# Optimization experiments

Hardware: AMD Instinct MI355X
Metric: run time of the kernel (lower is better)

## Reference

```python
import jax, jax.numpy as jnp
import numpy as np
import math

V, S, D, B = 50257, 2048, 512, 4
DFF = 4 * D
EPS = 1e-5


def layer_norm(z, g, b):
    mu = jnp.mean(z, axis=-1, keepdims=True)
    var = jnp.mean((z - mu) ** 2, axis=-1, keepdims=True)
    return (z - mu) * jax.lax.rsqrt(var + EPS) * g + b


def pos_embedding(seq_len, d_model):
    # Faithful to get_positional_value: angle = pos / 10000**(2*i/d), sin for even i, cos for odd i
    pos = jnp.arange(seq_len, dtype=jnp.float32)[:, None]          # [S,1]
    i = jnp.arange(d_model, dtype=jnp.float32)[None, :]            # [1,D]
    ang = pos / jnp.power(10000.0, 2.0 * i / d_model)              # [S,D]
    even = (jnp.arange(d_model) % 2 == 0)[None, :]
    return jnp.where(even, jnp.sin(ang), jnp.cos(ang))


def setup_inputs() -> dict:
    key = jax.random.key(0)
    ks = jax.random.split(key, 14)
    w = lambda k, sh: jax.random.normal(k, sh, dtype=jnp.float32) * 0.02
    return {
        "input_seq": jax.random.randint(ks[0], (B, S), 0, V),
        "emb": w(ks[1], (V, D)),
        "wk": w(ks[2], (D, D)), "bk": jnp.zeros((D,), jnp.float32),
        "wq": w(ks[3], (D, D)), "bq": jnp.zeros((D,), jnp.float32),
        "wv": w(ks[4], (D, D)), "bv": jnp.zeros((D,), jnp.float32),
        "ln_g": jnp.ones((D,), jnp.float32), "ln_b": jnp.zeros((D,), jnp.float32),
        "w1": w(ks[5], (D, DFF)), "b1": jnp.zeros((DFF,), jnp.float32),
        "w2": w(ks[6], (DFF, D)), "b2": jnp.zeros((D,), jnp.float32),
    }


def reference(input_seq, emb, wk, bk, wq, bq, wv, bv, ln_g, ln_b, w1, b1, w2, b2):
    x = emb[input_seq]                                              # [B,S,D]
    x = (x + pos_embedding(S, D)) * math.sqrt(D)
    # NB original passes (k, q, v) into Attention(Q, K, V), so Q:=k_proj, K:=q_proj, V:=v_proj
    k = x @ wk + bk
    q = x @ wq + bq
    v = x @ wv + bv
    scores = jnp.einsum("bid,bjd->bij", k, q) / math.sqrt(D)        # [B,S,S]
    attn = jax.nn.softmax(scores, axis=-1) @ v                      # [B,S,D]
    r = layer_norm(x + attn, ln_g, ln_b)
    ff = jax.nn.gelu(r @ w1 + b1, approximate=False) @ w2 + b2
    out = layer_norm(r + ff, ln_g, ln_b)                            # shared LN params (same module reused)
    return out
```

## Files before the change

kernel.cpp:

```cpp
#include <hip/hip_runtime.h>
#include <math.h>

static constexpr int BB  = 4;
static constexpr int S   = 2048;
static constexpr int D   = 512;
static constexpr int DFF = 2048;
static constexpr int BS  = BB * S;

using v8h = __attribute__((ext_vector_type(8))) _Float16;
using v4h = __attribute__((ext_vector_type(4))) _Float16;
using v2h = __attribute__((ext_vector_type(2))) _Float16;
using v4f = __attribute__((ext_vector_type(4))) float;

__device__ __forceinline__ void async16(const void* g, void* l) {
  __builtin_amdgcn_global_load_lds(
      (const __attribute__((address_space(1))) unsigned int*)g,
      (__attribute__((address_space(3))) unsigned int*)l, 16, 0, 0);
}

__device__ __forceinline__ void xcd_swizzle(int& bx, int& by) {
  const int nx = gridDim.x;
  const int nwg = nx * gridDim.y;
  const int lin = by * nx + bx;
  const int q = nwg >> 3;
  const int nl = (lin & 7) * q + (lin >> 3);
  bx = nl % nx;
  by = nl / nx;
}

__device__ __forceinline__ float fast_gelu(float v) {
  const float u = 0.7071067811865476f * v;
  const float a = fabsf(u);
  const float t = 1.0f / (1.0f + 0.3275911f * a);
  const float p =
      t * (0.254829592f +
           t * (-0.284496736f +
                t * (1.421413741f + t * (-1.453152027f + t * 1.061405429f))));
  const float e = exp2f(-u * u * 1.4426950408889634f);
  const float erfv = copysignf(1.0f - p * e, u);
  return 0.5f * v * (1.0f + erfv);
}

__device__ __forceinline__ float blockSum(float v) {
#pragma unroll
  for (int o = 32; o; o >>= 1) v += __shfl_xor(v, o, 64);
  __shared__ float t[4];
  __syncthreads();
  if ((threadIdx.x & 63) == 0) t[threadIdx.x >> 6] = v;
  __syncthreads();
  return t[0] + t[1] + t[2] + t[3];
}
__device__ __forceinline__ float blockMax(float v) {
#pragma unroll
  for (int o = 32; o; o >>= 1) v = fmaxf(v, __shfl_xor(v, o, 64));
  __shared__ float t[4];
  __syncthreads();
  if ((threadIdx.x & 63) == 0) t[threadIdx.x >> 6] = v;
  __syncthreads();
  return fmaxf(fmaxf(t[0], t[1]), fmaxf(t[2], t[3]));
}

__global__ __launch_bounds__(256) void embed_pos_k(
    const int* __restrict__ seq, const float* __restrict__ emb,
    float* __restrict__ X, _Float16* __restrict__ Xh) {
  const int bs = blockIdx.x;
  const int s  = bs & (S - 1);
  const int idx = seq[bs];
  const float* er = emb + (size_t)idx * D;
  const float cexp = -0.05190512648261504f;
  const int d0 = threadIdx.x * 2;
  const float2 e2 = *(const float2*)&er[d0];
  const float a0 = (float)s * exp2f((float)d0 * cexp);
  const float a1 = (float)s * exp2f((float)(d0 + 1) * cexp);
  const float v0 = (e2.x + sinf(a0)) * 22.62741699796952f;
  const float v1 = (e2.y + cosf(a1)) * 22.62741699796952f;
  const size_t o = (size_t)bs * D + d0;
  *(float2*)&X[o] = make_float2(v0, v1);
  *(v2h*)&Xh[o] = v2h{(_Float16)v0, (_Float16)v1};
}

__global__ __launch_bounds__(256) void prep_k(
    const float* __restrict__ wk, const float* __restrict__ wq,
    const float* __restrict__ wv, const float* __restrict__ w1,
    const float* __restrict__ w2, const float* __restrict__ bk,
    const float* __restrict__ bq, const float* __restrict__ bv,
    _Float16* __restrict__ wcat, _Float16* __restrict__ w1T,
    _Float16* __restrict__ w2T, float* __restrict__ bcat) {
  const int idx = blockIdx.x * 256 + threadIdx.x;
  if (idx < 786432) {
    const int which = idx >> 18, e = idx & 262143;
    const int k = e >> 9, n = e & 511;
    const float* w = (which == 0) ? wk : (which == 1) ? wq : wv;
    wcat[((long)(which * 512 + n)) * 512 + k] = (_Float16)w[e];
  } else if (idx < 786432 + 1048576) {
    const int e = idx - 786432;
    const int k = e >> 11, n = e & 2047;
    w1T[(long)n * 512 + k] = (_Float16)w1[e];
  } else if (idx < 786432 + 2097152) {
    const int e = idx - 786432 - 1048576;
    const int k = e >> 9, n = e & 511;
    w2T[(long)n * 2048 + k] = (_Float16)w2[e];
  } else if (idx < 786432 + 2097152 + 1536) {
    const int e = idx - 786432 - 2097152;
    const float* b = (e < 512) ? bk : (e < 1024) ? bq : bv;
    bcat[e] = b[e & 511];
  }
}

template <int OMODE, int ACT>
__global__ __launch_bounds__(256) void mm32_k(
    const _Float16* __restrict__ Ap, const _Float16* __restrict__ Bp,
    void* __restrict__ Cp, void* __restrict__ Cp2, void* __restrict__ Cp3,
    const float* __restrict__ bias,
    int N, int K, long sA, long sB, long sC, float scale) {
  constexpr int ATE = 128 * 32;
  constexpr int TILE = 2 * ATE;
  __shared__ __align__(16) _Float16 lds[2 * TILE];

  const int tid = threadIdx.x, lane = tid & 63, w = tid >> 6;
  const int quad = lane >> 4, l16 = lane & 15;
  const int wm = w >> 1, wn = w & 1;
  int bx = blockIdx.x, by = blockIdx.y;
  xcd_swizzle(bx, by);
  const int m0 = by * 128, n0 = bx * 128;

  const _Float16* A = Ap + (long)blockIdx.z * sA;
  const _Float16* B = Bp + (long)blockIdx.z * sB;

  v4f acc[4][4] = {};
  const int rloc = lane >> 2;
  const int cs = (lane & 3) ^ ((rloc >> 1) & 3);

  auto stage = [&](int k0, int half) {
    _Float16* Ah = lds + half * TILE;
    _Float16* Bh = Ah + ATE;
#pragma unroll
    for (int i = 0; i < 2; ++i) {
      const int is = w + i * 4;
      async16(A + (long)(m0 + is * 16 + rloc) * K + k0 + cs * 8, Ah + is * 512);
      async16(B + (long)(n0 + is * 16 + rloc) * K + k0 + cs * 8, Bh + is * 512);
    }
  };

  stage(0, 0);
  __syncthreads();

  const int nK = K >> 5;
  for (int t = 0; t < nK; ++t) {
    const int cur = t & 1;
    if (t + 1 < nK) stage((t + 1) << 5, cur ^ 1);

    const _Float16* Ah = lds + cur * TILE;
    const _Float16* Bh = Ah + ATE;

    v8h af[4], bfr[4];
#pragma unroll
    for (int mt = 0; mt < 4; ++mt) {
      const int rr = wm * 64 + mt * 16 + l16;
      const int pc = quad ^ ((rr >> 1) & 3);
      af[mt] = *(v8h*)&Ah[rr * 32 + pc * 8];
    }
#pragma unroll
    for (int nt = 0; nt < 4; ++nt) {
      const int rn = wn * 64 + nt * 16 + l16;
      const int pc = quad ^ ((rn >> 1) & 3);
      bfr[nt] = *(v8h*)&Bh[rn * 32 + pc * 8];
    }
#pragma unroll
    for (int mt = 0; mt < 4; ++mt)
#pragma unroll
      for (int nt = 0; nt < 4; ++nt)
        acc[mt][nt] = __builtin_amdgcn_mfma_f32_16x16x32_f16(
            af[mt], bfr[nt], acc[mt][nt], 0, 0, 0);

    __syncthreads();
  }

  const long Cz = (long)blockIdx.z * sC;
  const int region = n0 >> 9;
#pragma unroll
  for (int nt = 0; nt < 4; ++nt) {
    const int gn = n0 + wn * 64 + nt * 16 + l16;
    const int gnl = gn & 511;
    const float bv = bias ? bias[gn] : 0.0f;
#pragma unroll
    for (int mt = 0; mt < 4; ++mt) {
      const int gmb = m0 + wm * 64 + mt * 16 + quad * 4;
      if constexpr (OMODE == 4) {
        if (region == 2) {
          const int z2 = gmb >> 11, ml = gmb & 2047;
          v4h h4;
#pragma unroll
          for (int r = 0; r < 4; ++r)
            h4[r] = (_Float16)(acc[mt][nt][r] * scale + bv);
          *(v4h*)&((_Float16*)Cp3)[((long)z2 * 512 + gnl) * 2048 + ml] = h4;
          continue;
        }
      }
#pragma unroll
      for (int r = 0; r < 4; ++r) {
        const int gm = gmb + r;
        float v = acc[mt][nt][r] * scale + bv;
        if constexpr (ACT == 1) v = fast_gelu(v);
        if constexpr (OMODE == 0) {
          ((float*)Cp)[Cz + (long)gm * N + gn] = v;
        } else if constexpr (OMODE == 1) {
          ((_Float16*)Cp)[Cz + (long)gm * N + gn] = (_Float16)v;
        } else {
          if (region == 0) {
            ((_Float16*)Cp)[(long)gm * 512 + gnl] = (_Float16)v;
          } else {
            ((_Float16*)Cp2)[(long)gm * 512 + gnl] = (_Float16)v;
          }
        }
      }
    }
  }
}

template <int TM, int OMODE, int ACT>
__global__ __launch_bounds__(256) void mm_k(
    const _Float16* __restrict__ Ap, const _Float16* __restrict__ Bp,
    void* __restrict__ Cp, void* __restrict__ Cp2, void* __restrict__ Cp3,
    const float* __restrict__ bias,
    int N, int K, long sA, long sB, long sC, float scale) {
  constexpr int ATE = TM * 64;
  constexpr int BTE = 128 * 64;
  constexpr int TILE = ATE + BTE;
  __shared__ __align__(16) _Float16 lds[2 * TILE];

  const int tid = threadIdx.x, lane = tid & 63, w = tid >> 6;
  const int quad = lane >> 4, l16 = lane & 15;
  constexpr int MT = 4;
  constexpr int NT = (TM == 128) ? 4 : 2;
  constexpr int WN = (TM == 128) ? 64 : 32;
  const int wm = (TM == 128) ? (w >> 1) : 0;
  const int wn = (TM == 128) ? (w & 1) : w;
  int bx = blockIdx.x, by = blockIdx.y;
  xcd_swizzle(bx, by);
  const int m0 = by * TM, n0 = bx * 128;

  const _Float16* A = Ap + (long)blockIdx.z * sA;
  const _Float16* B = Bp + (long)blockIdx.z * sB;

  v4f acc[MT][NT] = {};
  const int srow8 = lane >> 3;
  const int cs = (lane & 7) ^ srow8;
  const int lsw = l16 & 7;

  auto stage = [&](int k0, int half) {
    _Float16* Ah = lds + half * TILE;
    _Float16* Bh = Ah + ATE;
#pragma unroll
    for (int i = 0; i < TM / 32; ++i) {
      const int is = w + i * 4;
      async16(A + (long)(m0 + is * 8 + srow8) * K + k0 + cs * 8, Ah + is * 512);
    }
#pragma unroll
    for (int i = 0; i < 4; ++i) {
      const int is = w + i * 4;
      async16(B + (long)(n0 + is * 8 + srow8) * K + k0 + cs * 8, Bh + is * 512);
    }
  };

  stage(0, 0);
  __syncthreads();

  const int nK = K >> 6;
  for (int t = 0; t < nK; ++t) {
    const int cur = t & 1;
    if (t + 1 < nK) stage((t + 1) << 6, cur ^ 1);

    const _Float16* Ah = lds + cur * TILE;
    const _Float16* Bh = Ah + ATE;

    v8h af[MT][2], bfr[NT][2];
#pragma unroll
    for (int mt = 0; mt < MT; ++mt) {
      const int rr = wm * 64 + mt * 16 + l16;
#pragma unroll
      for (int kk = 0; kk < 2; ++kk) {
        const int c = (kk * 4 + quad) ^ lsw;
        af[mt][kk] = *(v8h*)&Ah[rr * 64 + c * 8];
      }
    }
#pragma unroll
    for (int nt = 0; nt < NT; ++nt) {
      const int rn = wn * WN + nt * 16 + l16;
#pragma unroll
      for (int kk = 0; kk < 2; ++kk) {
        const int c = (kk * 4 + quad) ^ lsw;
        bfr[nt][kk] = *(v8h*)&Bh[rn * 64 + c * 8];
      }
    }
#pragma unroll
    for (int kk = 0; kk < 2; ++kk)
#pragma unroll
      for (int mt = 0; mt < MT; ++mt)
#pragma unroll
        for (int nt = 0; nt < NT; ++nt)
          acc[mt][nt] = __builtin_amdgcn_mfma_f32_16x16x32_f16(
              af[mt][kk], bfr[nt][kk], acc[mt][nt], 0, 0, 0);

    __syncthreads();
  }

  const long Cz = (long)blockIdx.z * sC;
#pragma unroll
  for (int nt = 0; nt < NT; ++nt) {
    const int gn = n0 + wn * WN + nt * 16 + l16;
    const float bv = bias ? bias[gn] : 0.0f;
#pragma unroll
    for (int mt = 0; mt < MT; ++mt) {
      const int gmb = m0 + wm * 64 + mt * 16 + quad * 4;
#pragma unroll
      for (int r = 0; r < 4; ++r) {
        const int gm = gmb + r;
        float v = acc[mt][nt][r] * scale + bv;
        if constexpr (ACT == 1) v = fast_gelu(v);
        if constexpr (OMODE == 0) {
          ((float*)Cp)[Cz + (long)gm * N + gn] = v;
        } else {
          ((_Float16*)Cp)[Cz + (long)gm * N + gn] = (_Float16)v;
        }
      }
    }
  }
}

__global__ __launch_bounds__(256) void mm64p_k(
    const _Float16* __restrict__ Ap, const _Float16* __restrict__ Bp,
    float* __restrict__ Cp, const float* __restrict__ bias,
    int N, int K, long sA, long sB, long sC, float scale) {
  constexpr int ATE = 64 * 64;
  constexpr int BTE = 128 * 64;
  constexpr int TILE = ATE + BTE;
  __shared__ __align__(16) _Float16 lds[3 * TILE];

  const int tid = threadIdx.x, lane = tid & 63, w = tid >> 6;
  const int quad = lane >> 4, l16 = lane & 15;
  int bx = blockIdx.x, by = blockIdx.y;
  xcd_swizzle(bx, by);
  const int m0 = by * 64, n0 = bx * 128;

  const _Float16* A = Ap + (long)blockIdx.z * sA;
  const _Float16* B = Bp + (long)blockIdx.z * sB;

  v4f acc[4][2] = {};
  const int srow8 = lane >> 3;
  const int cs = (lane & 7) ^ srow8;
  const int lsw = l16 & 7;

  auto stage = [&](int t) {
    _Float16* Ah = lds + (t % 3) * TILE;
    _Float16* Bh = Ah + ATE;
    const int k0 = t << 6;
#pragma unroll
    for (int i = 0; i < 2; ++i) {
      const int is = w + i * 4;
      async16(A + (long)(m0 + is * 8 + srow8) * K + k0 + cs * 8, Ah + is * 512);
    }
#pragma unroll
    for (int i = 0; i < 4; ++i) {
      const int is = w + i * 4;
      async16(B + (long)(n0 + is * 8 + srow8) * K + k0 + cs * 8, Bh + is * 512);
    }
  };

  const int nK = K >> 6;
  stage(0);
  stage(1);

  for (int t = 0; t < nK; ++t) {
    __builtin_amdgcn_s_barrier();
    if (t + 2 < nK) {
      stage(t + 2);
      asm volatile("s_waitcnt vmcnt(12)" ::: "memory");
    } else if (t + 1 < nK) {
      asm volatile("s_waitcnt vmcnt(6)" ::: "memory");
    } else {
      asm volatile("s_waitcnt vmcnt(0)" ::: "memory");
    }
    __builtin_amdgcn_s_barrier();

    const _Float16* Ah = lds + (t % 3) * TILE;
    const _Float16* Bh = Ah + ATE;

    v8h af[4][2], bfr[2][2];
#pragma unroll
    for (int mt = 0; mt < 4; ++mt) {
      const int rr = mt * 16 + l16;
#pragma unroll
      for (int kk = 0; kk < 2; ++kk) {
        const int c = (kk * 4 + quad) ^ lsw;
        af[mt][kk] = *(v8h*)&Ah[rr * 64 + c * 8];
      }
    }
#pragma unroll
    for (int nt = 0; nt < 2; ++nt) {
      const int rn = w * 32 + nt * 16 + l16;
#pragma unroll
      for (int kk = 0; kk < 2; ++kk) {
        const int c = (kk * 4 + quad) ^ lsw;
        bfr[nt][kk] = *(v8h*)&Bh[rn * 64 + c * 8];
      }
    }
#pragma unroll
    for (int kk = 0; kk < 2; ++kk)
#pragma unroll
      for (int mt = 0; mt < 4; ++mt)
#pragma unroll
        for (int nt = 0; nt < 2; ++nt)
          acc[mt][nt] = __builtin_amdgcn_mfma_f32_16x16x32_f16(
              af[mt][kk], bfr[nt][kk], acc[mt][nt], 0, 0, 0);
  }

  const long Cz = (long)blockIdx.z * sC;
#pragma unroll
  for (int nt = 0; nt < 2; ++nt) {
    const int gn = n0 + w * 32 + nt * 16 + l16;
    const float bv = bias ? bias[gn] : 0.0f;
#pragma unroll
    for (int mt = 0; mt < 4; ++mt) {
      const int gmb = m0 + mt * 16 + quad * 4;
#pragma unroll
      for (int r = 0; r < 4; ++r) {
        const int gm = gmb + r;
        Cp[Cz + (long)gm * N + gn] = acc[mt][nt][r] * scale + bv;
      }
    }
  }
}

__global__ __launch_bounds__(256) void softmax_k(_Float16* __restrict__ Sc) {
  _Float16* p = Sc + (size_t)blockIdx.x * S;
  const int base = threadIdx.x * 8;
  const v8h a = *(const v8h*)(p + base);
  float v[8];
#pragma unroll
  for (int i = 0; i < 8; ++i) v[i] = (float)a[i];
  float m = -1e30f;
#pragma unroll
  for (int i = 0; i < 8; ++i) m = fmaxf(m, v[i]);
  m = blockMax(m);
  float sum = 0.f;
#pragma unroll
  for (int i = 0; i < 8; ++i) {
    v[i] = exp2f((v[i] - m) * 1.44269504f);
    sum += v[i];
  }
  sum = blockSum(sum);
  const float inv = 1.0f / sum;
  v8h o;
#pragma unroll
  for (int i = 0; i < 8; ++i) o[i] = (_Float16)(v[i] * inv);
  *(v8h*)(p + base) = o;
}

__global__ __launch_bounds__(256) void ln_res_k(
    float* __restrict__ X, const float* __restrict__ Add,
    const float* __restrict__ g, const float* __restrict__ b,
    _Float16* __restrict__ rF) {
  float* xr = X + (size_t)blockIdx.x * D;
  const float* ar = Add + (size_t)blockIdx.x * D;
  _Float16* rf = rF + (size_t)blockIdx.x * D;
  const int d0 = threadIdx.x * 2;
  const float2 xv = *(const float2*)&xr[d0];
  const float2 av = *(const float2*)&ar[d0];
  const float z0 = xv.x + av.x;
  const float z1 = xv.y + av.y;
  const float mu = blockSum(z0 + z1) * (1.0f / D);
  const float dd0 = z0 - mu, dd1 = z1 - mu;
  const float var = blockSum(dd0 * dd0 + dd1 * dd1) * (1.0f / D);
  const float rs = rsqrtf(var + 1e-5f);
  const float2 gv = *(const float2*)&g[d0];
  const float2 bv = *(const float2*)&b[d0];
  const float v0 = dd0 * rs * gv.x + bv.x;
  const float v1 = dd1 * rs * gv.y + bv.y;
  *(float2*)&xr[d0] = make_float2(v0, v1);
  *(v2h*)&rf[d0] = v2h{(_Float16)v0, (_Float16)v1};
}

__global__ __launch_bounds__(256) void ln_out_k(
    const float* __restrict__ R, const float* __restrict__ F,
    const float* __restrict__ g, const float* __restrict__ b,
    float* __restrict__ out) {
  const float* rr = R + (size_t)blockIdx.x * D;
  const float* fr = F + (size_t)blockIdx.x * D;
  float* orow = out + (size_t)blockIdx.x * D;
  const int d0 = threadIdx.x * 2;
  const float2 rv = *(const float2*)&rr[d0];
  const float2 fv = *(const float2*)&fr[d0];
  const float z0 = rv.x + fv.x;
  const float z1 = rv.y + fv.y;
  const float mu = blockSum(z0 + z1) * (1.0f / D);
  const float dd0 = z0 - mu, dd1 = z1 - mu;
  const float var = blockSum(dd0 * dd0 + dd1 * dd1) * (1.0f / D);
  const float rs = rsqrtf(var + 1e-5f);
  const float2 gv = *(const float2*)&g[d0];
  const float2 bv = *(const float2*)&b[d0];
  *(float2*)&orow[d0] =
      make_float2(dd0 * rs * gv.x + bv.x, dd1 * rs * gv.y + bv.y);
}

extern "C" void kernel_launch(void* const* d_in, const int* in_sizes, int n_in,
                              void* d_out, int out_size, void* d_ws, size_t ws_size,
                              hipStream_t stream) {
  (void)in_sizes; (void)n_in; (void)out_size; (void)ws_size;
  const int*   seq = (const int*)d_in[0];
  const float* emb = (const float*)d_in[1];
  const float* wk  = (const float*)d_in[2];
  const float* bk  = (const float*)d_in[3];
  const float* wq  = (const float*)d_in[4];
  const float* bq  = (const float*)d_in[5];
  const float* wv  = (const float*)d_in[6];
  const float* bv  = (const float*)d_in[7];
  const float* lng = (const float*)d_in[8];
  const float* lnb = (const float*)d_in[9];
  const float* w1  = (const float*)d_in[10];
  const float* b1  = (const float*)d_in[11];
  const float* w2  = (const float*)d_in[12];
  const float* b2  = (const float*)d_in[13];

  const size_t MBy = 1024 * 1024;
  char* wsb = (char*)d_ws;
  float*    X    = (float*)wsb;
  _Float16* Xh   = (_Float16*)(wsb + 16 * MBy);
  _Float16* kF   = (_Float16*)(wsb + 24 * MBy);
  _Float16* qF   = (_Float16*)(wsb + 32 * MBy);
  _Float16* vT   = (_Float16*)(wsb + 40 * MBy);
  _Float16* Sc   = (_Float16*)(wsb + 48 * MBy);
  float*    attn = (float*)(wsb + 81 * MBy);
  _Float16* rF   = (_Float16*)(wsb + 24 * MBy);
  _Float16* hF   = (_Float16*)(wsb + 48 * MBy);
  float*    ff   = (float*)(wsb + 32 * MBy);
  _Float16* wcat = (_Float16*)(wsb + 100 * MBy);
  float*    bcat = (float*)(wsb + 102 * MBy);
  _Float16* w1T  = (_Float16*)(wsb + 103 * MBy);
  _Float16* w2T  = (_Float16*)(wsb + 105 * MBy);

  const long SD = (long)S * D, SSl = (long)S * S;

  prep_k<<<11270, 256, 0, stream>>>(wk, wq, wv, w1, w2, bk, bq, bv,
                                    wcat, w1T, w2T, bcat);
  embed_pos_k<<<BS, 256, 0, stream>>>(seq, emb, X, Xh);

  mm32_k<4, 0><<<dim3(12, 64, 1), 256, 0, stream>>>(
      Xh, wcat, kF, qF, vT, bcat, 1536, D, 0, 0, 0, 1.0f);

  mm32_k<1, 0><<<dim3(16, 16, BB), 256, 0, stream>>>(
      kF, qF, Sc, nullptr, nullptr, nullptr, S, D, SD, SD, SSl,
      0.044194173824159216f);

  softmax_k<<<BS, 256, 0, stream>>>(Sc);

  mm64p_k<<<dim3(4, 32, BB), 256, 0, stream>>>(
      Sc, vT, attn, nullptr, D, S, SSl, (long)D * S, SD, 1.0f);

  ln_res_k<<<BS, 256, 0, stream>>>(X, attn, lng, lnb, rF);

  mm32_k<1, 1><<<dim3(16, 64, 1), 256, 0, stream>>>(
      rF, w1T, hF, nullptr, nullptr, b1, DFF, D, 0, 0, 0, 1.0f);
  mm64p_k<<<dim3(4, 128, 1), 256, 0, stream>>>(
      hF, w2T, ff, b2, D, DFF, 0, 0, 0, 1.0f);

  ln_out_k<<<BS, 256, 0, stream>>>(X, ff, lng, lnb, (float*)d_out);
}
```

Before: 351.6 us.

## Fuse softmax into PV matmul with online max/sum rescaling

```diff
diff --git a/kernel.cpp b/kernel.cpp
--- a/kernel.cpp
+++ b/kernel.cpp
@@ -202,140 +202,31 @@
         const int gm = gmb + r;
         float v = acc[mt][nt][r] * scale + bv;
         if constexpr (ACT == 1) v = fast_gelu(v);
-        if constexpr (OMODE == 0) {
-          ((float*)Cp)[Cz + (long)gm * N + gn] = v;
-        } else if constexpr (OMODE == 1) {
+        if constexpr (OMODE == 1) {
           ((_Float16*)Cp)[Cz + (long)gm * N + gn] = (_Float16)v;
-        } else {
+        } else if constexpr (OMODE == 4) {
           if (region == 0) {
             ((_Float16*)Cp)[(long)gm * 512 + gnl] = (_Float16)v;
           } else {
             ((_Float16*)Cp2)[(long)gm * 512 + gnl] = (_Float16)v;
           }
+        } else {
+          ((float*)Cp)[Cz + (long)gm * N + gn] = v;
         }
       }
     }
   }
 }
 
-template <int TM, int OMODE, int ACT>
-__global__ __launch_bounds__(256) void mm_k(
+__global__ __launch_bounds__(256) void pv_sm_k(
     const _Float16* __restrict__ Ap, const _Float16* __restrict__ Bp,
-    void* __restrict__ Cp, void* __restrict__ Cp2, void* __restrict__ Cp3,
-    const float* __restrict__ bias,
-    int N, int K, long sA, long sB, long sC, float scale) {
-  constexpr int ATE = TM * 64;
-  constexpr int BTE = 128 * 64;
-  constexpr int TILE = ATE + BTE;
-  __shared__ __align__(16) _Float16 lds[2 * TILE];
-
-  const int tid = threadIdx.x, lane = tid & 63, w = tid >> 6;
-  const int quad = lane >> 4, l16 = lane & 15;
-  constexpr int MT = 4;
-  constexpr int NT = (TM == 128) ? 4 : 2;
-  constexpr int WN = (TM == 128) ? 64 : 32;
-  const int wm = (TM == 128) ? (w >> 1) : 0;
-  const int wn = (TM == 128) ? (w & 1) : w;
-  int bx = blockIdx.x, by = blockIdx.y;
-  xcd_swizzle(bx, by);
-  const int m0 = by * TM, n0 = bx * 128;
-
-  const _Float16* A = Ap + (long)blockIdx.z * sA;
-  const _Float16* B = Bp + (long)blockIdx.z * sB;
-
-  v4f acc[MT][NT] = {};
-  const int srow8 = lane >> 3;
-  const int cs = (lane & 7) ^ srow8;
-  const int lsw = l16 & 7;
-
-  auto stage = [&](int k0, int half) {
-    _Float16* Ah = lds + half * TILE;
-    _Float16* Bh = Ah + ATE;
-#pragma unroll
-    for (int i = 0; i < TM / 32; ++i) {
-      const int is = w + i * 4;
-      async16(A + (long)(m0 + is * 8 + srow8) * K + k0 + cs * 8, Ah + is * 512);
-    }
-#pragma unroll
-    for (int i = 0; i < 4; ++i) {
-      const int is = w + i * 4;
-      async16(B + (long)(n0 + is * 8 + srow8) * K + k0 + cs * 8, Bh + is * 512);
-    }
-  };
-
-  stage(0, 0);
-  __syncthreads();
-
-  const int nK = K >> 6;
-  for (int t = 0; t < nK; ++t) {
-    const int cur = t & 1;
-    if (t + 1 < nK) stage((t + 1) << 6, cur ^ 1);
-
-    const _Float16* Ah = lds + cur * TILE;
-    const _Float16* Bh = Ah + ATE;
-
-    v8h af[MT][2], bfr[NT][2];
-#pragma unroll
-    for (int mt = 0; mt < MT; ++mt) {
-      const int rr = wm * 64 + mt * 16 + l16;
-#pragma unroll
-      for (int kk = 0; kk < 2; ++kk) {
-        const int c = (kk * 4 + quad) ^ lsw;
-        af[mt][kk] = *(v8h*)&Ah[rr * 64 + c * 8];
-      }
-    }
-#pragma unroll
-    for (int nt = 0; nt < NT; ++nt) {
-      const int rn = wn * WN + nt * 16 + l16;
-#pragma unroll
-      for (int kk = 0; kk < 2; ++kk) {
-        const int c = (kk * 4 + quad) ^ lsw;
-        bfr[nt][kk] = *(v8h*)&Bh[rn * 64 + c * 8];
-      }
-    }
-#pragma unroll
-    for (int kk = 0; kk < 2; ++kk)
-#pragma unroll
-      for (int mt = 0; mt < MT; ++mt)
-#pragma unroll
-        for (int nt = 0; nt < NT; ++nt)
-          acc[mt][nt] = __builtin_amdgcn_mfma_f32_16x16x32_f16(
-              af[mt][kk], bfr[nt][kk], acc[mt][nt], 0, 0, 0);
-
-    __syncthreads();
-  }
-
-  const long Cz = (long)blockIdx.z * sC;
-#pragma unroll
-  for (int nt = 0; nt < NT; ++nt) {
-    const int gn = n0 + wn * WN + nt * 16 + l16;
-    const float bv = bias ? bias[gn] : 0.0f;
-#pragma unroll
-    for (int mt = 0; mt < MT; ++mt) {
-      const int gmb = m0 + wm * 64 + mt * 16 + quad * 4;
-#pragma unroll
-      for (int r = 0; r < 4; ++r) {
-        const int gm = gmb + r;
-        float v = acc[mt][nt][r] * scale + bv;
-        if constexpr (ACT == 1) v = fast_gelu(v);
-        if constexpr (OMODE == 0) {
-          ((float*)Cp)[Cz + (long)gm * N + gn] = v;
-        } else {
-          ((_Float16*)Cp)[Cz + (long)gm * N + gn] = (_Float16)v;
-        }
-      }
-    }
-  }
-}
-
-__global__ __launch_bounds__(256) void mm64p_k(
-    const _Float16* __restrict__ Ap, const _Float16* __restrict__ Bp,
-    float* __restrict__ Cp, const float* __restrict__ bias,
-    int N, int K, long sA, long sB, long sC, float scale) {
+    float* __restrict__ Cp,
+    int N, int K, long sA, long sB, long sC) {
   constexpr int ATE = 64 * 64;
   constexpr int BTE = 128 * 64;
   constexpr int TILE = ATE + BTE;
   __shared__ __align__(16) _Float16 lds[3 * TILE];
+  __shared__ __align__(16) float mS[64], lS[64], rS[64];
 
   const int tid = threadIdx.x, lane = tid & 63, w = tid >> 6;
   const int quad = lane >> 4, l16 = lane & 15;
@@ -346,10 +237,13 @@
   const _Float16* A = Ap + (long)blockIdx.z * sA;
   const _Float16* B = Bp + (long)blockIdx.z * sB;
 
+  if (tid < 64) { mS[tid] = -1e30f; lS[tid] = 0.0f; }
+
   v4f acc[4][2] = {};
   const int srow8 = lane >> 3;
   const int cs = (lane & 7) ^ srow8;
   const int lsw = l16 & 7;
+  const float L2E = 1.44269504f;
 
   auto stage = [&](int t) {
     _Float16* Ah = lds + (t % 3) * TILE;
@@ -405,6 +299,175 @@
         bfr[nt][kk] = *(v8h*)&Bh[rn * 64 + c * 8];
       }
     }
+
+    float tmax[4];
+#pragma unroll
+    for (int mt = 0; mt < 4; ++mt) {
+      float tm = -1e30f;
+#pragma unroll
+      for (int kk = 0; kk < 2; ++kk)
+#pragma unroll
+        for (int j = 0; j < 8; ++j)
+          tm = fmaxf(tm, (float)af[mt][kk][j]);
+      tm = fmaxf(tm, __shfl_xor(tm, 16, 64));
+      tm = fmaxf(tm, __shfl_xor(tm, 32, 64));
+      tmax[mt] = tm;
+    }
+    if (w == 0 && quad == 0) {
+#pragma unroll
+      for (int mt = 0; mt < 4; ++mt) {
+        const int rr = mt * 16 + l16;
+        const float mo = mS[rr];
+        const float mn = fmaxf(mo, tmax[mt]);
+        rS[rr] = exp2f((mo - mn) * L2E);
+        mS[rr] = mn;
+      }
+    }
+    asm volatile("s_waitcnt lgkmcnt(0)" ::: "memory");
+    __builtin_amdgcn_s_barrier();
+
+    v8h paf[4][2];
+    float ts[4];
+#pragma unroll
+    for (int mt = 0; mt < 4; ++mt) {
+      const int rr = mt * 16 + l16;
+      const float mn = mS[rr];
+      float s = 0.f;
+#pragma unroll
+      for (int kk = 0; kk < 2; ++kk)
+#pragma unroll
+        for (int j = 0; j < 8; ++j) {
+          const float p = exp2f(((float)af[mt][kk][j] - mn) * L2E);
+          s += p;
+          paf[mt][kk][j] = (_Float16)p;
+        }
+      s += __shfl_xor(s, 16, 64);
+      s += __shfl_xor(s, 32, 64);
+      ts[mt] = s;
+    }
+    if (w == 0 && quad == 0) {
+#pragma unroll
+      for (int mt = 0; mt < 4; ++mt) {
+        const int rr = mt * 16 + l16;
+        lS[rr] = lS[rr] * rS[rr] + ts[mt];
+      }
+    }
+
+#pragma unroll
+    for (int mt = 0; mt < 4; ++mt) {
+      const v4f r4 = *(const v4f*)&rS[mt * 16 + quad * 4];
+#pragma unroll
+      for (int nt = 0; nt < 2; ++nt)
+#pragma unroll
+        for (int r = 0; r < 4; ++r)
+          acc[mt][nt][r] *= r4[r];
+    }
+
+#pragma unroll
+    for (int kk = 0; kk < 2; ++kk)
+#pragma unroll
+      for (int mt = 0; mt < 4; ++mt)
+#pragma unroll
+        for (int nt = 0; nt < 2; ++nt)
+          acc[mt][nt] = __builtin_amdgcn_mfma_f32_16x16x32_f16(
+              paf[mt][kk], bfr[nt][kk], acc[mt][nt], 0, 0, 0);
+  }
+
+  asm volatile("s_waitcnt lgkmcnt(0)" ::: "memory");
+  __builtin_amdgcn_s_barrier();
+
+  const long Cz = (long)blockIdx.z * sC;
+#pragma unroll
+  for (int nt = 0; nt < 2; ++nt) {
+    const int gn = n0 + w * 32 + nt * 16 + l16;
+#pragma unroll
+    for (int mt = 0; mt < 4; ++mt) {
+      const int gmb = m0 + mt * 16 + quad * 4;
+      const v4f l4 = *(const v4f*)&lS[mt * 16 + quad * 4];
+#pragma unroll
+      for (int r = 0; r < 4; ++r)
+        Cp[Cz + (long)(gmb + r) * N + gn] = acc[mt][nt][r] / l4[r];
+    }
+  }
+}
+
+__global__ __launch_bounds__(256) void mm64p_k(
+    const _Float16* __restrict__ Ap, const _Float16* __restrict__ Bp,
+    float* __restrict__ Cp, const float* __restrict__ bias,
+    int N, int K, long sA, long sB, long sC, float scale) {
+  constexpr int ATE = 64 * 64;
+  constexpr int BTE = 128 * 64;
+  constexpr int TILE = ATE + BTE;
+  __shared__ __align__(16) _Float16 lds[3 * TILE];
+
+  const int tid = threadIdx.x, lane = tid & 63, w = tid >> 6;
+  const int quad = lane >> 4, l16 = lane & 15;
+  int bx = blockIdx.x, by = blockIdx.y;
+  xcd_swizzle(bx, by);
+  const int m0 = by * 64, n0 = bx * 128;
+
+  const _Float16* A = Ap + (long)blockIdx.z * sA;
+  const _Float16* B = Bp + (long)blockIdx.z * sB;
+
+  v4f acc[4][2] = {};
+  const int srow8 = lane >> 3;
+  const int cs = (lane & 7) ^ srow8;
+  const int lsw = l16 & 7;
+
+  auto stage = [&](int t) {
+    _Float16* Ah = lds + (t % 3) * TILE;
+    _Float16* Bh = Ah + ATE;
+    const int k0 = t << 6;
+#pragma unroll
+    for (int i = 0; i < 2; ++i) {
+      const int is = w + i * 4;
+      async16(A + (long)(m0 + is * 8 + srow8) * K + k0 + cs * 8, Ah + is * 512);
+    }
+#pragma unroll
+    for (int i = 0; i < 4; ++i) {
+      const int is = w + i * 4;
+      async16(B + (long)(n0 + is * 8 + srow8) * K + k0 + cs * 8, Bh + is * 512);
+    }
+  };
+
+  const int nK = K >> 6;
+  stage(0);
+  stage(1);
+
+  for (int t = 0; t < nK; ++t) {
+    __builtin_amdgcn_s_barrier();
+    if (t + 2 < nK) {
+      stage(t + 2);
+      asm volatile("s_waitcnt vmcnt(12)" ::: "memory");
+    } else if (t + 1 < nK) {
+      asm volatile("s_waitcnt vmcnt(6)" ::: "memory");
+    } else {
+      asm volatile("s_waitcnt vmcnt(0)" ::: "memory");
+    }
+    __builtin_amdgcn_s_barrier();
+
+    const _Float16* Ah = lds + (t % 3) * TILE;
+    const _Float16* Bh = Ah + ATE;
+
+    v8h af[4][2], bfr[2][2];
+#pragma unroll
+    for (int mt = 0; mt < 4; ++mt) {
+      const int rr = mt * 16 + l16;
+#pragma unroll
+      for (int kk = 0; kk < 2; ++kk) {
+        const int c = (kk * 4 + quad) ^ lsw;
+        af[mt][kk] = *(v8h*)&Ah[rr * 64 + c * 8];
+      }
+    }
+#pragma unroll
+    for (int nt = 0; nt < 2; ++nt) {
+      const int rn = w * 32 + nt * 16 + l16;
+#pragma unroll
+      for (int kk = 0; kk < 2; ++kk) {
+        const int c = (kk * 4 + quad) ^ lsw;
+        bfr[nt][kk] = *(v8h*)&Bh[rn * 64 + c * 8];
+      }
+    }
 #pragma unroll
     for (int kk = 0; kk < 2; ++kk)
 #pragma unroll
@@ -430,31 +493,6 @@
       }
     }
   }
-}
-
-__global__ __launch_bounds__(256) void softmax_k(_Float16* __restrict__ Sc) {
-  _Float16* p = Sc + (size_t)blockIdx.x * S;
-  const int base = threadIdx.x * 8;
-  const v8h a = *(const v8h*)(p + base);
-  float v[8];
-#pragma unroll
-  for (int i = 0; i < 8; ++i) v[i] = (float)a[i];
-  float m = -1e30f;
-#pragma unroll
-  for (int i = 0; i < 8; ++i) m = fmaxf(m, v[i]);
-  m = blockMax(m);
-  float sum = 0.f;
-#pragma unroll
-  for (int i = 0; i < 8; ++i) {
-    v[i] = exp2f((v[i] - m) * 1.44269504f);
-    sum += v[i];
-  }
-  sum = blockSum(sum);
-  const float inv = 1.0f / sum;
-  v8h o;
-#pragma unroll
-  for (int i = 0; i < 8; ++i) o[i] = (_Float16)(v[i] * inv);
-  *(v8h*)(p + base) = o;
 }
 
 __global__ __launch_bounds__(256) void ln_res_k(
@@ -552,10 +590,8 @@
       kF, qF, Sc, nullptr, nullptr, nullptr, S, D, SD, SD, SSl,
       0.044194173824159216f);
 
-  softmax_k<<<BS, 256, 0, stream>>>(Sc);
-
-  mm64p_k<<<dim3(4, 32, BB), 256, 0, stream>>>(
-      Sc, vT, attn, nullptr, D, S, SSl, (long)D * S, SD, 1.0f);
+  pv_sm_k<<<dim3(4, 32, BB), 256, 0, stream>>>(
+      Sc, vT, attn, D, S, SSl, (long)D * S, SD);
 
   ln_res_k<<<BS, 256, 0, stream>>>(X, attn, lng, lnb, rF);
 
```

New measurement: 453.7 us. +29.0%, slower.
